# Kernel optimization log

Measured on AMD Instinct MI355X. Metric: run time of the kernel, lower is better.

Reference implementation:

```python
import jax, jax.numpy as jnp
import numpy as np

N_NODES = 100000
N_EDGES = 3200000
HIDDEN = 64
NUM_LABELS = 1000
NUM_GRAPHS = 128


def setup_inputs() -> dict:
    key = jax.random.key(0)
    ks = jax.random.split(key, 12)
    node_labels = jax.random.randint(ks[0], (N_NODES,), 0, NUM_LABELS)
    edge_index = jax.random.randint(ks[1], (2, N_EDGES), 0, N_NODES)
    edge_weight = jax.random.uniform(ks[2], (N_EDGES,), dtype=jnp.float32)
    batch = jnp.sort(jax.random.randint(ks[3], (N_NODES,), 0, NUM_GRAPHS))
    s = 1.0 / np.sqrt(HIDDEN)
    emb = jax.random.normal(ks[4], (NUM_LABELS, HIDDEN), dtype=jnp.float32)
    W1 = jax.random.normal(ks[5], (HIDDEN, HIDDEN), dtype=jnp.float32) * s
    b1 = jnp.zeros((HIDDEN,), dtype=jnp.float32)
    W2 = jax.random.normal(ks[6], (HIDDEN, HIDDEN), dtype=jnp.float32) * s
    b2 = jnp.zeros((HIDDEN,), dtype=jnp.float32)
    W3 = jax.random.normal(ks[7], (HIDDEN, HIDDEN), dtype=jnp.float32) * s
    b3 = jnp.zeros((HIDDEN,), dtype=jnp.float32)
    W4 = jax.random.normal(ks[8], (HIDDEN, 1), dtype=jnp.float32) * s
    b4 = jnp.zeros((1,), dtype=jnp.float32)
    return {"node_labels": node_labels, "edge_index": edge_index,
            "edge_weight": edge_weight, "batch": batch, "emb": emb,
            "W1": W1, "b1": b1, "W2": W2, "b2": b2,
            "W3": W3, "b3": b3, "W4": W4, "b4": b4}


def _gcn_conv(x, W, b, src, dst, ew):
    # PyG GCNConv: add self-loops (weight 1), symmetric D^-1/2 normalization.
    h = x @ W                                               # [N, H]
    deg = jax.ops.segment_sum(ew, dst, num_segments=N_NODES) + 1.0  # self-loop
    dinv = jax.lax.rsqrt(deg)                               # [N]
    norm = dinv[src] * ew * dinv[dst]                       # [E]
    out = jax.ops.segment_sum(h[src] * norm[:, None], dst, num_segments=N_NODES)
    out = out + h * (dinv * dinv)[:, None]                  # self-loop message
    return out + b


def reference(node_labels, edge_index, edge_weight, batch, emb,
              W1, b1, W2, b2, W3, b3, W4, b4):
    src, dst = edge_index[0], edge_index[1]
    x = emb[node_labels]                                    # [N, H]
    x = jax.nn.relu(_gcn_conv(x, W1, b1, src, dst, edge_weight))
    x = jax.nn.relu(_gcn_conv(x, W2, b2, src, dst, edge_weight))
    # global mean pool over graphs (dropout is identity in eval mode)
    sums = jax.ops.segment_sum(x, batch, num_segments=NUM_GRAPHS)   # [G, H]
    cnts = jax.ops.segment_sum(jnp.ones((N_NODES,), x.dtype), batch,
                               num_segments=NUM_GRAPHS)
    g = sums / jnp.maximum(cnts, 1.0)[:, None]
    g = jax.nn.relu(g @ W3 + b3)
    return jnp.squeeze(g @ W4 + b4, axis=-1)                # [G]
```

## Files before the change

### kernel.cpp

```cpp
#include <hip/hip_runtime.h>
#include <hip/hip_fp16.h>

#define N_NODES    100000
#define N_EDGES    3200000
#define HIDDEN     64
#define NUM_GRAPHS 128
#define NUM_LABELS 1000

#define BKT_SHIFT  8
#define NPB        256
#define NBKT       ((N_NODES + NPB - 1) / NPB)
#define ENTCAP     8960
#define BSLOT      ENTCAP
#define SCHUNK     4096
#define SNBLK      ((N_EDGES + SCHUNK - 1) / SCHUNK)
#define CPT        ((SNBLK + 255) / 256)

__global__ __launch_bounds__(256) void hist_blk_kernel(
    const int* __restrict__ dst, int* __restrict__ cnt, int E) {
    __shared__ int h[NBKT];
    int t = threadIdx.x;
    for (int b = t; b < NBKT; b += 256) h[b] = 0;
    __syncthreads();
    int base = blockIdx.x * SCHUNK;
    int end  = min(base + SCHUNK, E);
    for (int i = base + t; i < end; i += 256)
        atomicAdd(&h[dst[i] >> BKT_SHIFT], 1);
    __syncthreads();
    int* o = cnt + (size_t)blockIdx.x * NBKT;
    for (int b = t; b < NBKT; b += 256) o[b] = h[b];
}

__global__ __launch_bounds__(256) void scan_cols_kernel(
    const int* __restrict__ cnt, int* __restrict__ basem, int* __restrict__ bktTot) {
    __shared__ int a[256], bsh[256];
    int b = blockIdx.x;
    int t = threadIdx.x;
    int v[CPT];
    int loc = 0;
    int blk0 = t * CPT;
    #pragma unroll
    for (int j = 0; j < CPT; ++j) {
        int blk = blk0 + j;
        int c = (blk < SNBLK) ? cnt[(size_t)blk * NBKT + b] : 0;
        v[j] = loc;
        loc += c;
    }
    a[t] = loc; __syncthreads();
    int* pa = a; int* pb = bsh;
    #pragma unroll
    for (int d = 1; d < 256; d <<= 1) {
        int x = pa[t];
        if (t >= d) x += pa[t - d];
        pb[t] = x; __syncthreads();
        int* tmp = pa; pa = pb; pb = tmp;
    }
    int ex = (t == 0) ? 0 : pa[t - 1];
    #pragma unroll
    for (int j = 0; j < CPT; ++j) {
        int blk = blk0 + j;
        if (blk < SNBLK) basem[(size_t)blk * NBKT + b] = ex + v[j];
    }
    if (t == 255) bktTot[b] = pa[255];
}

__global__ __launch_bounds__(512) void scan_buckets_kernel(const int* __restrict__ bktTot,
                                                           int* __restrict__ boff) {
    __shared__ int a[512], b[512];
    int t = threadIdx.x;
    int v = (t < NBKT) ? bktTot[t] : 0;
    a[t] = v; __syncthreads();
    int* pa = a; int* pb = b;
    #pragma unroll
    for (int d = 1; d < 512; d <<= 1) {
        int x = pa[t];
        if (t >= d) x += pa[t - d];
        pb[t] = x; __syncthreads();
        int* tmp = pa; pa = pb; pb = tmp;
    }
    int ex = (t == 0) ? 0 : pa[t - 1];
    if (t < NBKT) boff[t] = ex;
    if (t == NBKT - 1) boff[NBKT] = pa[t];
}

__global__ __launch_bounds__(256) void scatter_kernel(
    const int* __restrict__ src, const int* __restrict__ dst,
    const float* __restrict__ ew, const int* __restrict__ basem,
    int2* __restrict__ barr, int E) {
    __shared__ int h[NBKT];
    __shared__ int wb[NBKT];
    int t = threadIdx.x;
    const int* bm = basem + (size_t)blockIdx.x * NBKT;
    for (int b = t; b < NBKT; b += 256) { h[b] = 0; wb[b] = bm[b]; }
    __syncthreads();
    int base = blockIdx.x * SCHUNK;
    int end  = min(base + SCHUNK, E);
    for (int i = base + t; i < end; i += 256) {
        int d  = dst[i];
        int bk = d >> BKT_SHIFT;
        int p  = atomicAdd(&h[bk], 1);
        barr[(size_t)bk * BSLOT + wb[bk] + p] =
            make_int2(src[i] | ((d & (NPB - 1)) << 20), __float_as_int(ew[i]));
    }
}

__global__ __launch_bounds__(256) void finalize_kernel(
    const int2* __restrict__ barr, const int* __restrict__ boff,
    const int* __restrict__ labels,
    int2* __restrict__ csr, int* __restrict__ off, float* __restrict__ dinv) {
    __shared__ int2  ent[ENTCAP];
    __shared__ int   hcnt[NPB];
    __shared__ float wsum[NPB];
    __shared__ float ldv[NPB];
    __shared__ int   ha[NPB], hcur[NPB];
    int b = blockIdx.x;
    int t = threadIdx.x;
    int s = boff[b], e = boff[b + 1];
    int m = e - s;
    const int2* bsrc = barr + (size_t)b * BSLOT;
    int node0 = b << BKT_SHIFT;
    int nn = min(NPB, N_NODES - node0);
    if (t < NPB) { hcnt[t] = 0; wsum[t] = 0.f; }
    __syncthreads();
    bool staged = (m <= ENTCAP);
    for (int i = t; i < m; i += 256) {
        int2 v = bsrc[i];
        if (staged) ent[i] = v;
        int doff = (v.x >> 20) & (NPB - 1);
        atomicAdd(&hcnt[doff], 1);
        atomicAdd(&wsum[doff], __int_as_float(v.y));
    }
    __syncthreads();
    ha[t] = hcnt[t];
    __syncthreads();
    #pragma unroll
    for (int d = 1; d < NPB; d <<= 1) {
        int x = ha[t];
        if (t >= d) x += ha[t - d];
        __syncthreads();
        ha[t] = x;
        __syncthreads();
    }
    {
        int ex = (t == 0) ? 0 : ha[t - 1];
        hcur[t] = s + ex;
        float dv = rsqrtf(wsum[t] + 1.0f);
        ldv[t] = dv;
        if (t < nn) {
            off[node0 + t]  = s + ex;
            dinv[node0 + t] = dv;
        }
    }
    if (b == NBKT - 1 && t == 0) off[N_NODES] = e;
    __syncthreads();
    for (int i = t; i < m; i += 256) {
        int2 v = staged ? ent[i] : bsrc[i];
        int doff = (v.x >> 20) & (NPB - 1);
        int sv   = v.x & 0xFFFFF;
        float wf = __int_as_float(v.y) * ldv[doff];
        int lab  = labels[sv];
        int p = atomicAdd(&hcur[doff], 1);
        csr[p] = make_int2(sv | (lab << 17), __float_as_int(wf));
    }
}

__global__ __launch_bounds__(256) void ew1_kernel(
    const float* __restrict__ emb, const float* __restrict__ W,
    __half* __restrict__ OUTH) {
    __shared__ float Ws[64 * 64];
    __shared__ float Xs[64 * 65];
    int t = threadIdx.x;
    #pragma unroll
    for (int s = 0; s < 16; ++s) Ws[s * 256 + t] = W[s * 256 + t];
    int r0   = blockIdx.x * 64;
    int lrow = t >> 2;
    int c0   = (t & 3) * 16;
    int grow = r0 + lrow;
    const float* srcrow = (grow < NUM_LABELS) ? (emb + (size_t)grow * HIDDEN) : emb;
    #pragma unroll
    for (int c = 0; c < 16; c += 4) {
        float4 v = *(const float4*)(srcrow + c0 + c);
        Xs[lrow * 65 + c0 + c + 0] = v.x;
        Xs[lrow * 65 + c0 + c + 1] = v.y;
        Xs[lrow * 65 + c0 + c + 2] = v.z;
        Xs[lrow * 65 + c0 + c + 3] = v.w;
    }
    __syncthreads();
    int row = t & 63;
    int j0  = (t >> 6) * 16;
    float4 a0 = make_float4(0,0,0,0), a1 = a0, a2 = a0, a3 = a0;
    #pragma unroll
    for (int k = 0; k < 64; ++k) {
        float xv = Xs[row * 65 + k];
        const float4* wr = (const float4*)(Ws + k * 64 + j0);
        float4 w0 = wr[0], w1 = wr[1], w2 = wr[2], w3 = wr[3];
        a0.x = fmaf(xv, w0.x, a0.x); a0.y = fmaf(xv, w0.y, a0.y);
        a0.z = fmaf(xv, w0.z, a0.z); a0.w = fmaf(xv, w0.w, a0.w);
        a1.x = fmaf(xv, w1.x, a1.x); a1.y = fmaf(xv, w1.y, a1.y);
        a1.z = fmaf(xv, w1.z, a1.z); a1.w = fmaf(xv, w1.w, a1.w);
        a2.x = fmaf(xv, w2.x, a2.x); a2.y = fmaf(xv, w2.y, a2.y);
        a2.z = fmaf(xv, w2.z, a2.z); a2.w = fmaf(xv, w2.w, a2.w);
        a3.x = fmaf(xv, w3.x, a3.x); a3.y = fmaf(xv, w3.y, a3.y);
        a3.z = fmaf(xv, w3.z, a3.z); a3.w = fmaf(xv, w3.w, a3.w);
    }
    int gr = r0 + row;
    if (gr < NUM_LABELS) {
        union { __half2 h2[8]; uint4 u4[2]; } pk;
        pk.h2[0] = __floats2half2_rn(a0.x, a0.y);
        pk.h2[1] = __floats2half2_rn(a0.z, a0.w);
        pk.h2[2] = __floats2half2_rn(a1.x, a1.y);
        pk.h2[3] = __floats2half2_rn(a1.z, a1.w);
        pk.h2[4] = __floats2half2_rn(a2.x, a2.y);
        pk.h2[5] = __floats2half2_rn(a2.z, a2.w);
        pk.h2[6] = __floats2half2_rn(a3.x, a3.y);
        pk.h2[7] = __floats2half2_rn(a3.z, a3.w);
        uint4* o = (uint4*)(OUTH + (size_t)gr * HIDDEN + j0);
        o[0] = pk.u4[0]; o[1] = pk.u4[1];
    }
}

#define ACC8(rv_, wv_) { \
    const __half2* hp_ = (const __half2*)&(rv_); \
    float2 f0_ = __half22float2(hp_[0]); \
    float2 f1_ = __half22float2(hp_[1]); \
    float2 f2_ = __half22float2(hp_[2]); \
    float2 f3_ = __half22float2(hp_[3]); \
    accA.x = fmaf(f0_.x, (wv_), accA.x); accA.y = fmaf(f0_.y, (wv_), accA.y); \
    accA.z = fmaf(f1_.x, (wv_), accA.z); accA.w = fmaf(f1_.y, (wv_), accA.w); \
    accB.x = fmaf(f2_.x, (wv_), accB.x); accB.y = fmaf(f2_.y, (wv_), accB.y); \
    accB.z = fmaf(f3_.x, (wv_), accB.z); accB.w = fmaf(f3_.y, (wv_), accB.w); }

#define RED8(of_) { \
    accA.x += __shfl_xor(accA.x, of_, 64); accA.y += __shfl_xor(accA.y, of_, 64); \
    accA.z += __shfl_xor(accA.z, of_, 64); accA.w += __shfl_xor(accA.w, of_, 64); \
    accB.x += __shfl_xor(accB.x, of_, 64); accB.y += __shfl_xor(accB.y, of_, 64); \
    accB.z += __shfl_xor(accB.z, of_, 64); accB.w += __shfl_xor(accB.w, of_, 64); }

__global__ __launch_bounds__(256) void agg1_kernel(
    const __half* __restrict__ EW1h, const int* __restrict__ labels,
    const int2* __restrict__ csr, const int* __restrict__ off,
    const float* __restrict__ dinv, const float* __restrict__ bias,
    __half* __restrict__ A1h, int n) {
    int wid  = (blockIdx.x * blockDim.x + threadIdx.x) >> 6;
    if (wid >= n) return;
    int lane = threadIdx.x & 63;
    int q = lane & 7, g = lane >> 3;
    int i   = off[wid] + g;
    int end = off[wid + 1];
    float4 accA = make_float4(0.f,0.f,0.f,0.f), accB = accA;
    while (i < end) {
        int2 e0 = csr[i];
        int2 e1 = (i + 8  < end) ? csr[i + 8]  : make_int2(0, 0);
        int2 e2 = (i + 16 < end) ? csr[i + 16] : make_int2(0, 0);
        int2 e3 = (i + 24 < end) ? csr[i + 24] : make_int2(0, 0);
        uint4 r0 = *(const uint4*)(EW1h + (size_t)((unsigned)e0.x >> 17) * HIDDEN + q * 8);
        uint4 r1 = *(const uint4*)(EW1h + (size_t)((unsigned)e1.x >> 17) * HIDDEN + q * 8);
        uint4 r2 = *(const uint4*)(EW1h + (size_t)((unsigned)e2.x >> 17) * HIDDEN + q * 8);
        uint4 r3 = *(const uint4*)(EW1h + (size_t)((unsigned)e3.x >> 17) * HIDDEN + q * 8);
        float w0 = __int_as_float(e0.y) * dinv[e0.x & 0x1FFFF];
        float w1 = __int_as_float(e1.y) * dinv[e1.x & 0x1FFFF];
        float w2 = __int_as_float(e2.y) * dinv[e2.x & 0x1FFFF];
        float w3 = __int_as_float(e3.y) * dinv[e3.x & 0x1FFFF];
        ACC8(r0, w0); ACC8(r1, w1); ACC8(r2, w2); ACC8(r3, w3);
        i += 32;
    }
    RED8(8); RED8(16); RED8(32);
    if (g == 0) {
        float di  = dinv[wid];
        float di2 = di * di;
        int labw = labels[wid];
        uint4 xu = *(const uint4*)(EW1h + (size_t)labw * HIDDEN + q * 8);
        const __half2* xp = (const __half2*)&xu;
        float2 x0 = __half22float2(xp[0]);
        float2 x1 = __half22float2(xp[1]);
        float2 x2 = __half22float2(xp[2]);
        float2 x3 = __half22float2(xp[3]);
        const float4* bp = (const float4*)(bias + q * 8);
        float4 bv0 = bp[0], bv1 = bp[1];
        float4 vA, vB;
        vA.x = fmaxf(fmaf(x0.x, di2, accA.x) + bv0.x, 0.f);
        vA.y = fmaxf(fmaf(x0.y, di2, accA.y) + bv0.y, 0.f);
        vA.z = fmaxf(fmaf(x1.x, di2, accA.z) + bv0.z, 0.f);
        vA.w = fmaxf(fmaf(x1.y, di2, accA.w) + bv0.w, 0.f);
        vB.x = fmaxf(fmaf(x2.x, di2, accB.x) + bv1.x, 0.f);
        vB.y = fmaxf(fmaf(x2.y, di2, accB.y) + bv1.y, 0.f);
        vB.z = fmaxf(fmaf(x3.x, di2, accB.z) + bv1.z, 0.f);
        vB.w = fmaxf(fmaf(x3.y, di2, accB.w) + bv1.w, 0.f);
        union { __half2 h2[4]; uint4 u4; } pk;
        pk.h2[0] = __floats2half2_rn(vA.x, vA.y);
        pk.h2[1] = __floats2half2_rn(vA.z, vA.w);
        pk.h2[2] = __floats2half2_rn(vB.x, vB.y);
        pk.h2[3] = __floats2half2_rn(vB.z, vB.w);
        *(uint4*)(A1h + (size_t)wid * HIDDEN + q * 8) = pk.u4;
    }
}

__global__ __launch_bounds__(256) void agg2_kernel(
    const __half* __restrict__ Xh,
    const int2* __restrict__ csr, const int* __restrict__ off,
    const float* __restrict__ dinv, float* __restrict__ OUT, int n) {
    int wid  = (blockIdx.x * blockDim.x + threadIdx.x) >> 6;
    if (wid >= n) return;
    int lane = threadIdx.x & 63;
    int q = lane & 7, g = lane >> 3;
    int i   = off[wid] + g;
    int end = off[wid + 1];
    float4 accA = make_float4(0.f,0.f,0.f,0.f), accB = accA;
    while (i < end) {
        int2 e0 = csr[i];
        int2 e1 = (i + 8  < end) ? csr[i + 8]  : make_int2(0, 0);
        int2 e2 = (i + 16 < end) ? csr[i + 16] : make_int2(0, 0);
        int2 e3 = (i + 24 < end) ? csr[i + 24] : make_int2(0, 0);
        uint4 r0 = *(const uint4*)(Xh + (size_t)(e0.x & 0x1FFFF) * HIDDEN + q * 8);
        uint4 r1 = *(const uint4*)(Xh + (size_t)(e1.x & 0x1FFFF) * HIDDEN + q * 8);
        uint4 r2 = *(const uint4*)(Xh + (size_t)(e2.x & 0x1FFFF) * HIDDEN + q * 8);
        uint4 r3 = *(const uint4*)(Xh + (size_t)(e3.x & 0x1FFFF) * HIDDEN + q * 8);
        float w0 = __int_as_float(e0.y) * dinv[e0.x & 0x1FFFF];
        float w1 = __int_as_float(e1.y) * dinv[e1.x & 0x1FFFF];
        float w2 = __int_as_float(e2.y) * dinv[e2.x & 0x1FFFF];
        float w3 = __int_as_float(e3.y) * dinv[e3.x & 0x1FFFF];
        ACC8(r0, w0); ACC8(r1, w1); ACC8(r2, w2); ACC8(r3, w3);
        i += 32;
    }
    RED8(8); RED8(16); RED8(32);
    if (g == 0) {
        float di  = dinv[wid];
        float di2 = di * di;
        uint4 xu = *(const uint4*)(Xh + (size_t)wid * HIDDEN + q * 8);
        const __half2* xp = (const __half2*)&xu;
        float2 x0 = __half22float2(xp[0]);
        float2 x1 = __half22float2(xp[1]);
        float2 x2 = __half22float2(xp[2]);
        float2 x3 = __half22float2(xp[3]);
        accA.x = fmaf(x0.x, di2, accA.x);
        accA.y = fmaf(x0.y, di2, accA.y);
        accA.z = fmaf(x1.x, di2, accA.z);
        accA.w = fmaf(x1.y, di2, accA.w);
        accB.x = fmaf(x2.x, di2, accB.x);
        accB.y = fmaf(x2.y, di2, accB.y);
        accB.z = fmaf(x3.x, di2, accB.z);
        accB.w = fmaf(x3.y, di2, accB.w);
        float* o = OUT + (size_t)wid * HIDDEN + q * 8;
        *(float4*)o       = accA;
        *(float4*)(o + 4) = accB;
    }
}

__global__ __launch_bounds__(256) void gemm2_kernel(
    const float* __restrict__ X, const float* __restrict__ W,
    const float* __restrict__ bias, float* __restrict__ OUT, int n) {
    __shared__ float Ws[64 * 64];
    __shared__ float Xs[64 * 65];
    int t = threadIdx.x;
    #pragma unroll
    for (int s = 0; s < 16; ++s) Ws[s * 256 + t] = W[s * 256 + t];
    int r0   = blockIdx.x * 64;
    int lrow = t >> 2;
    int c0   = (t & 3) * 16;
    const float* srcrow = ((r0 + lrow) < n) ? (X + (size_t)(r0 + lrow) * HIDDEN) : X;
    #pragma unroll
    for (int c = 0; c < 16; c += 4) {
        float4 v = *(const float4*)(srcrow + c0 + c);
        Xs[lrow * 65 + c0 + c + 0] = v.x;
        Xs[lrow * 65 + c0 + c + 1] = v.y;
        Xs[lrow * 65 + c0 + c + 2] = v.z;
        Xs[lrow * 65 + c0 + c + 3] = v.w;
    }
    __syncthreads();
    int row = t & 63;
    int j0  = (t >> 6) * 16;
    float4 a0 = *(const float4*)(bias + j0 + 0);
    float4 a1 = *(const float4*)(bias + j0 + 4);
    float4 a2 = *(const float4*)(bias + j0 + 8);
    float4 a3 = *(const float4*)(bias + j0 + 12);
    #pragma unroll
    for (int k = 0; k < 64; ++k) {
        float xv = Xs[row * 65 + k];
        const float4* wr = (const float4*)(Ws + k * 64 + j0);
        float4 w0 = wr[0], w1 = wr[1], w2 = wr[2], w3 = wr[3];
        a0.x = fmaf(xv, w0.x, a0.x); a0.y = fmaf(xv, w0.y, a0.y);
        a0.z = fmaf(xv, w0.z, a0.z); a0.w = fmaf(xv, w0.w, a0.w);
        a1.x = fmaf(xv, w1.x, a1.x); a1.y = fmaf(xv, w1.y, a1.y);
        a1.z = fmaf(xv, w1.z, a1.z); a1.w = fmaf(xv, w1.w, a1.w);
        a2.x = fmaf(xv, w2.x, a2.x); a2.y = fmaf(xv, w2.y, a2.y);
        a2.z = fmaf(xv, w2.z, a2.z); a2.w = fmaf(xv, w2.w, a2.w);
        a3.x = fmaf(xv, w3.x, a3.x); a3.y = fmaf(xv, w3.y, a3.y);
        a3.z = fmaf(xv, w3.z, a3.z); a3.w = fmaf(xv, w3.w, a3.w);
    }
    int gr = r0 + row;
    if (gr < n) {
        float4* o = (float4*)(OUT + (size_t)gr * HIDDEN + j0);
        a0.x = fmaxf(a0.x, 0.f); a0.y = fmaxf(a0.y, 0.f); a0.z = fmaxf(a0.z, 0.f); a0.w = fmaxf(a0.w, 0.f);
        a1.x = fmaxf(a1.x, 0.f); a1.y = fmaxf(a1.y, 0.f); a1.z = fmaxf(a1.z, 0.f); a1.w = fmaxf(a1.w, 0.f);
        a2.x = fmaxf(a2.x, 0.f); a2.y = fmaxf(a2.y, 0.f); a2.z = fmaxf(a2.z, 0.f); a2.w = fmaxf(a2.w, 0.f);
        a3.x = fmaxf(a3.x, 0.f); a3.y = fmaxf(a3.y, 0.f); a3.z = fmaxf(a3.z, 0.f); a3.w = fmaxf(a3.w, 0.f);
        o[0] = a0; o[1] = a1; o[2] = a2; o[3] = a3;
    }
}

__global__ __launch_bounds__(256) void pool_head_kernel(
    const float* __restrict__ A, const int* __restrict__ batch,
    const float* __restrict__ W3, const float* __restrict__ b3,
    const float* __restrict__ W4, const float* __restrict__ b4,
    float* __restrict__ out) {
    __shared__ int   sb[2];
    __shared__ float sd[4][64];
    __shared__ float gv[64];
    int gidx = blockIdx.x;
    int t = threadIdx.x;
    if (t < 2) {
        int target = gidx + t;
        int lo = 0, hi = N_NODES;
        while (lo < hi) {
            int mid = (lo + hi) >> 1;
            if (batch[mid] < target) lo = mid + 1; else hi = mid;
        }
        sb[t] = lo;
    }
    __syncthreads();
    int start = sb[0], end = sb[1];
    int col = t & 63, rg = t >> 6;
    float sum = 0.f;
    for (int r = start + rg; r < end; r += 4) sum += A[(size_t)r * HIDDEN + col];
    sd[rg][col] = sum;
    __syncthreads();
    if (t < 64) {
        float tot = sd[0][col] + sd[1][col] + sd[2][col] + sd[3][col];
        float cnt = (float)(end - start);
        gv[col] = tot / fmaxf(cnt, 1.0f);
    }
    __syncthreads();
    if (t < 64) {
        float acc = b3[t];
        #pragma unroll
        for (int k = 0; k < 64; ++k) acc = fmaf(gv[k], W3[k * 64 + t], acc);
        float p = fmaxf(acc, 0.f) * W4[t];
        #pragma unroll
        for (int o = 32; o > 0; o >>= 1) p += __shfl_down(p, o, 64);
        if (t == 0) out[gidx] = p + b4[0];
    }
}

extern "C" void kernel_launch(void* const* d_in, const int* in_sizes, int n_in,
                              void* d_out, int out_size, void* d_ws, size_t ws_size,
                              hipStream_t stream) {
    const int*   labels = (const int*)d_in[0];
    const int*   ei     = (const int*)d_in[1];
    const int*   src    = ei;
    const int*   dst    = ei + N_EDGES;
    const float* ew     = (const float*)d_in[2];
    const int*   batch  = (const int*)d_in[3];
    const float* emb    = (const float*)d_in[4];
    const float* W1 = (const float*)d_in[5],  *b1 = (const float*)d_in[6];
    const float* W2 = (const float*)d_in[7],  *b2 = (const float*)d_in[8];
    const float* W3 = (const float*)d_in[9],  *b3 = (const float*)d_in[10];
    const float* W4 = (const float*)d_in[11], *b4 = (const float*)d_in[12];
    float* out = (float*)d_out;

    float* ws   = (float*)d_ws;
    float* bufH = ws;
    float* bufA = bufH + (size_t)N_NODES * HIDDEN;
    int2*  csr  = (int2*)(bufA + (size_t)N_NODES * HIDDEN);
    int*   boff   = (int*)(csr + N_EDGES);
    int*   bktTot = boff + NBKT + 1;
    int*   off    = bktTot + NBKT;
    float* dinv   = (float*)(off + N_NODES + 1);
    __half* EW1h  = (__half*)(dinv + N_NODES);
    int2*  barr   = (int2*)ws;
    __half* A1h   = (__half*)bufA;
    float* A2     = bufA;
    int*   cnt    = (int*)csr;
    int*   basem  = cnt + (size_t)SNBLK * NBKT;

    const int NT = 256;
    const int blkW = (N_NODES * 64 + NT - 1) / NT;
    const int blkG = (N_NODES + 63) / 64;

    hist_blk_kernel<<<SNBLK, NT, 0, stream>>>(dst, cnt, N_EDGES);
    scan_cols_kernel<<<NBKT, NT, 0, stream>>>(cnt, basem, bktTot);
    scan_buckets_kernel<<<1, 512, 0, stream>>>(bktTot, boff);
    scatter_kernel<<<SNBLK, NT, 0, stream>>>(src, dst, ew, basem, barr, N_EDGES);
    finalize_kernel<<<NBKT, NT, 0, stream>>>(barr, boff, labels, csr, off, dinv);

    ew1_kernel<<<(NUM_LABELS + 63) / 64, NT, 0, stream>>>(emb, W1, EW1h);
    agg1_kernel<<<blkW, NT, 0, stream>>>(EW1h, labels, csr, off, dinv, b1, A1h, N_NODES);

    agg2_kernel<<<blkW, NT, 0, stream>>>(A1h, csr, off, dinv, bufH, N_NODES);
    gemm2_kernel<<<blkG, NT, 0, stream>>>(bufH, W2, b2, A2, N_NODES);

    pool_head_kernel<<<NUM_GRAPHS, NT, 0, stream>>>(A2, batch, W3, b3, W4, b4, out);
}
```

Before: 413.7 us.

## Stage scatter writes in LDS by bucket and fold source dinv into CSR weights

The scatter kernel now computes a per-block local prefix over bucket counts, stages entries in shared memory sorted by bucket, and then writes them out in bucket-contiguous order, so global writes coalesce better. A new dinv_bucket_kernel computes the degree normalisation before finalize, so finalize can multiply in the source node's dinv and store a fully normalised edge weight. This removes the random dinv gather per edge in both aggregation kernels. The cost is an extra kernel pass over the bucket array and a random dinv gather inside finalize.

Result: no change. 414.2 us (+0.1%).

```diff
diff --git a/kernel.cpp b/kernel.cpp
--- a/kernel.cpp
+++ b/kernel.cpp
@@ -85,32 +85,72 @@
 
 __global__ __launch_bounds__(256) void scatter_kernel(
     const int* __restrict__ src, const int* __restrict__ dst,
-    const float* __restrict__ ew, const int* __restrict__ basem,
-    int2* __restrict__ barr, int E) {
-    __shared__ int h[NBKT];
-    __shared__ int wb[NBKT];
-    int t = threadIdx.x;
-    const int* bm = basem + (size_t)blockIdx.x * NBKT;
-    for (int b = t; b < NBKT; b += 256) { h[b] = 0; wb[b] = bm[b]; }
-    __syncthreads();
-    int base = blockIdx.x * SCHUNK;
+    const float* __restrict__ ew, const int* __restrict__ cnt,
+    const int* __restrict__ basem, int2* __restrict__ barr, int E) {
+    __shared__ int2 ent[SCHUNK];
+    __shared__ int  gaddr[SCHUNK];
+    __shared__ int  h[NBKT];
+    __shared__ int  ls[NBKT];
+    __shared__ int  a[256], bsc[256];
+    int t = threadIdx.x;
+    int blk = blockIdx.x;
+    const int* cn = cnt   + (size_t)blk * NBKT;
+    const int* bm = basem + (size_t)blk * NBKT;
+    int i0 = 2 * t, i1 = 2 * t + 1;
+    int c0 = (i0 < NBKT) ? cn[i0] : 0;
+    int c1 = (i1 < NBKT) ? cn[i1] : 0;
+    a[t] = c0 + c1; __syncthreads();
+    int* pa = a; int* pb = bsc;
+    #pragma unroll
+    for (int d = 1; d < 256; d <<= 1) {
+        int x = pa[t];
+        if (t >= d) x += pa[t - d];
+        pb[t] = x; __syncthreads();
+        int* tmp = pa; pa = pb; pb = tmp;
+    }
+    int ex = (t == 0) ? 0 : pa[t - 1];
+    if (i0 < NBKT) { ls[i0] = ex;      h[i0] = 0; }
+    if (i1 < NBKT) { ls[i1] = ex + c0; h[i1] = 0; }
+    __syncthreads();
+    int base = blk * SCHUNK;
     int end  = min(base + SCHUNK, E);
+    int m    = end - base;
     for (int i = base + t; i < end; i += 256) {
         int d  = dst[i];
         int bk = d >> BKT_SHIFT;
         int p  = atomicAdd(&h[bk], 1);
-        barr[(size_t)bk * BSLOT + wb[bk] + p] =
-            make_int2(src[i] | ((d & (NPB - 1)) << 20), __float_as_int(ew[i]));
-    }
+        int j  = ls[bk] + p;
+        ent[j]   = make_int2(src[i] | ((d & (NPB - 1)) << 20), __float_as_int(ew[i]));
+        gaddr[j] = bk * BSLOT + bm[bk] + p;
+    }
+    __syncthreads();
+    for (int j = t; j < m; j += 256) barr[gaddr[j]] = ent[j];
+}
+
+__global__ __launch_bounds__(256) void dinv_bucket_kernel(
+    const int2* __restrict__ barr, const int* __restrict__ bktTot,
+    float* __restrict__ dinv) {
+    __shared__ float wsum[NPB];
+    int b = blockIdx.x, t = threadIdx.x;
+    wsum[t] = 0.f;
+    __syncthreads();
+    int m = bktTot[b];
+    const int2* bs = barr + (size_t)b * BSLOT;
+    for (int i = t; i < m; i += 256) {
+        int2 v = bs[i];
+        atomicAdd(&wsum[(v.x >> 20) & (NPB - 1)], __int_as_float(v.y));
+    }
+    __syncthreads();
+    int node = (b << BKT_SHIFT) + t;
+    if (node < N_NODES) dinv[node] = rsqrtf(wsum[t] + 1.0f);
 }
 
 __global__ __launch_bounds__(256) void finalize_kernel(
     const int2* __restrict__ barr, const int* __restrict__ boff,
-    const int* __restrict__ labels,
-    int2* __restrict__ csr, int* __restrict__ off, float* __restrict__ dinv) {
+    const int* __restrict__ labels, const float* __restrict__ dinv,
+    int2* __restrict__ csr, int* __restrict__ off) {
     __shared__ int2  ent[ENTCAP];
     __shared__ int   hcnt[NPB];
-    __shared__ float wsum[NPB];
     __shared__ float ldv[NPB];
     __shared__ int   ha[NPB], hcur[NPB];
     int b = blockIdx.x;
@@ -120,15 +160,14 @@
     const int2* bsrc = barr + (size_t)b * BSLOT;
     int node0 = b << BKT_SHIFT;
     int nn = min(NPB, N_NODES - node0);
-    if (t < NPB) { hcnt[t] = 0; wsum[t] = 0.f; }
+    hcnt[t] = 0;
+    ldv[t]  = (t < nn) ? dinv[node0 + t] : 0.f;
     __syncthreads();
     bool staged = (m <= ENTCAP);
     for (int i = t; i < m; i += 256) {
         int2 v = bsrc[i];
         if (staged) ent[i] = v;
-        int doff = (v.x >> 20) & (NPB - 1);
-        atomicAdd(&hcnt[doff], 1);
-        atomicAdd(&wsum[doff], __int_as_float(v.y));
+        atomicAdd(&hcnt[(v.x >> 20) & (NPB - 1)], 1);
     }
     __syncthreads();
     ha[t] = hcnt[t];
@@ -144,12 +183,7 @@
     {
         int ex = (t == 0) ? 0 : ha[t - 1];
         hcur[t] = s + ex;
-        float dv = rsqrtf(wsum[t] + 1.0f);
-        ldv[t] = dv;
-        if (t < nn) {
-            off[node0 + t]  = s + ex;
-            dinv[node0 + t] = dv;
-        }
+        if (t < nn) off[node0 + t] = s + ex;
     }
     if (b == NBKT - 1 && t == 0) off[N_NODES] = e;
     __syncthreads();
@@ -157,7 +191,7 @@
         int2 v = staged ? ent[i] : bsrc[i];
         int doff = (v.x >> 20) & (NPB - 1);
         int sv   = v.x & 0xFFFFF;
-        float wf = __int_as_float(v.y) * ldv[doff];
+        float wf = __int_as_float(v.y) * ldv[doff] * dinv[sv];
         int lab  = labels[sv];
         int p = atomicAdd(&hcur[doff], 1);
         csr[p] = make_int2(sv | (lab << 17), __float_as_int(wf));
@@ -257,10 +291,10 @@
         uint4 r1 = *(const uint4*)(EW1h + (size_t)((unsigned)e1.x >> 17) * HIDDEN + q * 8);
         uint4 r2 = *(const uint4*)(EW1h + (size_t)((unsigned)e2.x >> 17) * HIDDEN + q * 8);
         uint4 r3 = *(const uint4*)(EW1h + (size_t)((unsigned)e3.x >> 17) * HIDDEN + q * 8);
-        float w0 = __int_as_float(e0.y) * dinv[e0.x & 0x1FFFF];
-        float w1 = __int_as_float(e1.y) * dinv[e1.x & 0x1FFFF];
-        float w2 = __int_as_float(e2.y) * dinv[e2.x & 0x1FFFF];
-        float w3 = __int_as_float(e3.y) * dinv[e3.x & 0x1FFFF];
+        float w0 = __int_as_float(e0.y);
+        float w1 = __int_as_float(e1.y);
+        float w2 = __int_as_float(e2.y);
+        float w3 = __int_as_float(e3.y);
         ACC8(r0, w0); ACC8(r1, w1); ACC8(r2, w2); ACC8(r3, w3);
         i += 32;
     }
@@ -315,10 +349,10 @@
         uint4 r1 = *(const uint4*)(Xh + (size_t)(e1.x & 0x1FFFF) * HIDDEN + q * 8);
         uint4 r2 = *(const uint4*)(Xh + (size_t)(e2.x & 0x1FFFF) * HIDDEN + q * 8);
         uint4 r3 = *(const uint4*)(Xh + (size_t)(e3.x & 0x1FFFF) * HIDDEN + q * 8);
-        float w0 = __int_as_float(e0.y) * dinv[e0.x & 0x1FFFF];
-        float w1 = __int_as_float(e1.y) * dinv[e1.x & 0x1FFFF];
-        float w2 = __int_as_float(e2.y) * dinv[e2.x & 0x1FFFF];
-        float w3 = __int_as_float(e3.y) * dinv[e3.x & 0x1FFFF];
+        float w0 = __int_as_float(e0.y);
+        float w1 = __int_as_float(e1.y);
+        float w2 = __int_as_float(e2.y);
+        float w3 = __int_as_float(e3.y);
         ACC8(r0, w0); ACC8(r1, w1); ACC8(r2, w2); ACC8(r3, w3);
         i += 32;
     }
@@ -479,8 +513,9 @@
     hist_blk_kernel<<<SNBLK, NT, 0, stream>>>(dst, cnt, N_EDGES);
     scan_cols_kernel<<<NBKT, NT, 0, stream>>>(cnt, basem, bktTot);
     scan_buckets_kernel<<<1, 512, 0, stream>>>(bktTot, boff);
-    scatter_kernel<<<SNBLK, NT, 0, stream>>>(src, dst, ew, basem, barr, N_EDGES);
-    finalize_kernel<<<NBKT, NT, 0, stream>>>(barr, boff, labels, csr, off, dinv);
+    scatter_kernel<<<SNBLK, NT, 0, stream>>>(src, dst, ew, cnt, basem, barr, N_EDGES);
+    dinv_bucket_kernel<<<NBKT, NT, 0, stream>>>(barr, bktTot, dinv);
+    finalize_kernel<<<NBKT, NT, 0, stream>>>(barr, boff, labels, dinv, csr, off);
 
     ew1_kernel<<<(NUM_LABELS + 63) / 64, NT, 0, stream>>>(emb, W1, EW1h);
     agg1_kernel<<<blkW, NT, 0, stream>>>(EW1h, labels, csr, off, dinv, b1, A1h, N_NODES);
```
